# Performance work log

Measured on AMD Instinct MI355X. Metric: run time of the kernel, lower is better.

The kernel has to match this reference:

```python
import jax, jax.numpy as jnp
import numpy as np

N = 50000
E = 500000
R = 8
IN_DIM = 128
HID = 128
NUM_CLASSES = 16
NUM_GRAPHS = 64


def setup_inputs() -> dict:
    key = jax.random.key(0)
    ks = jax.random.split(key, 12)
    x = jax.random.normal(ks[0], (N, IN_DIM), dtype=jnp.float32)
    edge_index = jax.random.randint(ks[1], (2, E), 0, N)
    edge_type = jax.random.randint(ks[2], (E,), 0, R)
    batch = jnp.sort(jax.random.randint(ks[3], (N,), 0, NUM_GRAPHS))
    s = 1.0 / np.sqrt(IN_DIM)
    W1 = jax.random.uniform(ks[4], (R, IN_DIM, HID), minval=-s, maxval=s, dtype=jnp.float32)
    root1 = jax.random.uniform(ks[5], (IN_DIM, HID), minval=-s, maxval=s, dtype=jnp.float32)
    b1 = jnp.zeros((HID,), jnp.float32)
    s2 = 1.0 / np.sqrt(HID)
    W2 = jax.random.uniform(ks[6], (R, HID, HID), minval=-s2, maxval=s2, dtype=jnp.float32)
    root2 = jax.random.uniform(ks[7], (HID, HID), minval=-s2, maxval=s2, dtype=jnp.float32)
    b2 = jnp.zeros((HID,), jnp.float32)
    linW = jax.random.uniform(ks[8], (HID, NUM_CLASSES), minval=-s2, maxval=s2, dtype=jnp.float32)
    linb = jnp.zeros((NUM_CLASSES,), jnp.float32)
    return {"x": x, "edge_index": edge_index, "edge_type": edge_type, "batch": batch,
            "W1": W1, "root1": root1, "b1": b1, "W2": W2, "root2": root2, "b2": b2,
            "linW": linW, "linb": linb}


def rgcn_conv(x, src, dst, rel, W, root, b):
    # Per-relation transform of ALL nodes once: [R, N, H] (avoids per-edge weight gather)
    xW = jnp.einsum('nd,rdh->rnh', x, W)
    msg = xW[rel, src]                      # [E, H] gather per edge
    # PyG RGCNConv default aggr='mean': mean over neighbors per (dst, relation)
    seg = dst * R + rel                     # composite segment id
    cnt = jax.ops.segment_sum(jnp.ones((msg.shape[0],), msg.dtype), seg, num_segments=N * R)
    norm = 1.0 / jnp.maximum(cnt, 1.0)
    msg = msg * norm[seg][:, None]
    agg = jax.ops.segment_sum(msg, dst, num_segments=N)  # sum over relations folds in
    return agg + x @ root + b


def global_mean_pool(x, batch):
    sums = jax.ops.segment_sum(x, batch, num_segments=NUM_GRAPHS)
    cnt = jax.ops.segment_sum(jnp.ones((x.shape[0],), x.dtype), batch, num_segments=NUM_GRAPHS)
    return sums / jnp.maximum(cnt, 1.0)[:, None]


def reference(x, edge_index, edge_type, batch, W1, root1, b1, W2, root2, b2, linW, linb):
    src, dst = edge_index[0], edge_index[1]
    h = jax.nn.relu(rgcn_conv(x, src, dst, edge_type, W1, root1, b1))
    h = jax.nn.relu(rgcn_conv(h, src, dst, edge_type, W2, root2, b2))
    pooled = global_mean_pool(h, batch)     # [G, HID]
    return pooled @ linW + linb             # [G, NUM_CLASSES]
```

## Files before the change

### kernel.cpp

```cpp
#include <hip/hip_runtime.h>
#include <hip/hip_bf16.h>
#include <stdint.h>

#define N_NODES 50000
#define N_EDGES 500000
#define R_REL 8
#define HID 128
#define KIN 128
#define KOUT 1152
#define NUM_GRAPHS 64
#define NUM_CLASSES 16

#define BN 32
#define LDA 1160
#define NKC 36
#define NBLK 1563

typedef __attribute__((ext_vector_type(8))) short bf16x8;
typedef __attribute__((ext_vector_type(4))) float f32x4;

__device__ __forceinline__ uint16_t f2bf(float f) {
  uint32_t u = __float_as_uint(f);
  u += 0x7FFFu + ((u >> 16) & 1u);
  return (uint16_t)(u >> 16);
}
__device__ __forceinline__ float bf2f(uint32_t b) {
  return __uint_as_float(b << 16);
}
__device__ __forceinline__ uint32_t pack2bf(float a, float b) {
  return (uint32_t)f2bf(a) | ((uint32_t)f2bf(b) << 16);
}

#define HIST_B 1954
#define BND_B 196
#define PW_B 576
#define CVT_B 3125
__global__ __launch_bounds__(256) void k_prep(const int* __restrict__ ei, const int* __restrict__ et,
                                              int* __restrict__ deg,
                                              const int* __restrict__ batch,
                                              int* __restrict__ gs, int* __restrict__ ge,
                                              const float* __restrict__ W1, const float* __restrict__ root1,
                                              uint16_t* __restrict__ Wf1,
                                              const float* __restrict__ W2, const float* __restrict__ root2,
                                              uint16_t* __restrict__ Wf2,
                                              const float* __restrict__ x, uint16_t* __restrict__ xb) {
  int b = blockIdx.x;
  if (b < HIST_B) {
    int i = b * 256 + threadIdx.x;
    if (i < N_EDGES) atomicAdd(&deg[ei[N_EDGES + i]], 1);
    return;
  }
  b -= HIST_B;
  if (b < BND_B) {
    int i = b * 256 + threadIdx.x;
    if (i < N_NODES) {
      int g = batch[i];
      if (i == 0) gs[g] = 0;
      else { int pg = batch[i - 1]; if (pg != g) { ge[pg] = i; gs[g] = i; } }
      if (i == N_NODES - 1) ge[g] = N_NODES;
    }
    return;
  }
  b -= BND_B;
  if (b < 2 * PW_B) {
    const float* W    = (b < PW_B) ? W1 : W2;
    const float* root = (b < PW_B) ? root1 : root2;
    uint16_t*    Wf   = (b < PW_B) ? Wf1 : Wf2;
    int idx = (b % PW_B) * 256 + threadIdx.x;
    int e = idx & 7, L = (idx >> 3) & 63, f = idx >> 9;
    int quad = L >> 4, l16 = L & 15;
    int nt = f & 7, kc = f >> 3;
    int kk = kc * 32 + quad * 8 + e;
    int s = kk >> 7, k = kk & 127;
    int col = nt * 16 + l16;
    float v = (s < R_REL) ? W[((size_t)s * KIN + k) * HID + col] : root[(size_t)k * HID + col];
    Wf[idx] = f2bf(v);
    return;
  }
  b -= 2 * PW_B;
  {
    int i = b * 256 + threadIdx.x;
    const float4* p = (const float4*)x + (size_t)i * 2;
    float4 a = p[0], c = p[1];
    uint4 o;
    o.x = pack2bf(a.x, a.y); o.y = pack2bf(a.z, a.w);
    o.z = pack2bf(c.x, c.y); o.w = pack2bf(c.z, c.w);
    *(uint4*)(xb + (size_t)i * 8) = o;
  }
}

__global__ __launch_bounds__(256) void k_scan1(const int* __restrict__ deg, int* __restrict__ offs,
                                               int* __restrict__ bsum) {
  __shared__ int sh[256];
  int t = threadIdx.x;
  int base = blockIdx.x * 1024 + t * 4;
  int v[4]; int s = 0;
  #pragma unroll
  for (int i = 0; i < 4; ++i) { int idx = base + i; v[i] = (idx < N_NODES) ? deg[idx] : 0; s += v[i]; }
  sh[t] = s;
  __syncthreads();
  for (int d = 1; d < 256; d <<= 1) {
    int add = (t >= d) ? sh[t - d] : 0;
    __syncthreads();
    sh[t] += add;
    __syncthreads();
  }
  int run = sh[t] - s;
  if (t == 255) bsum[blockIdx.x] = sh[255];
  #pragma unroll
  for (int i = 0; i < 4; ++i) { int idx = base + i; if (idx < N_NODES) offs[idx] = run; run += v[i]; }
}

__global__ __launch_bounds__(512) void k_scan2(int* __restrict__ bsum, int nb) {
  __shared__ int sh[512];
  int t = threadIdx.x;
  int v = (t < nb) ? bsum[t] : 0;
  sh[t] = v;
  __syncthreads();
  for (int d = 1; d < 512; d <<= 1) {
    int add = (t >= d) ? sh[t - d] : 0;
    __syncthreads();
    sh[t] += add;
    __syncthreads();
  }
  if (t < nb) bsum[t] = sh[t] - v;
}

__global__ __launch_bounds__(256) void k_scan3(int* __restrict__ offs, int* __restrict__ nxt,
                                               const int* __restrict__ bsum) {
  int i = blockIdx.x * 256 + threadIdx.x;
  if (i < N_NODES) {
    int o = offs[i] + bsum[i >> 10];
    offs[i] = o;
    nxt[i] = o;
  }
  if (i == 0) offs[N_NODES] = N_EDGES;
}

__global__ __launch_bounds__(256) void k_scatter(const int* __restrict__ ei, const int* __restrict__ et,
                                                 int* __restrict__ nxt, uint32_t* __restrict__ epack) {
  int i = blockIdx.x * 256 + threadIdx.x;
  if (i < N_EDGES) {
    int rel = et[i];
    int key = ei[N_EDGES + i];
    int p = atomicAdd(&nxt[key], 1);
    epack[p] = (uint32_t)ei[i] | ((uint32_t)rel << 16);
  }
}

template<int MODE>
__global__ __launch_bounds__(512, 4) void k_fused(const uint16_t* __restrict__ hin,
                                                  const uint32_t* __restrict__ epack,
                                                  const int* __restrict__ offs,
                                                  const uint16_t* __restrict__ Wf,
                                                  const float* __restrict__ bias,
                                                  void* __restrict__ hout,
                                                  float* __restrict__ psum,
                                                  const int* __restrict__ batch) {
  __shared__ __align__(16) uint16_t As[BN * LDA];
  int t = threadIdx.x;
  int w = __builtin_amdgcn_readfirstlane(t >> 6);
  int L = t & 63;
  int quad = L >> 4, l16 = L & 15;
  int node0 = blockIdx.x * BN;

  {
    bf16x8 z = 0;
    #pragma unroll
    for (int i = 0; i < 9; ++i) ((bf16x8*)As)[i * 512 + t] = z;
    if (t < 32) ((bf16x8*)As)[9 * 512 + t] = z;
  }

  int offv = offs[min(node0 + min(L, 32), N_NODES)];

  const uint16_t* wp = Wf + (size_t)w * 512 + (size_t)L * 8;
  bf16x8 b0 = *(const bf16x8*)(wp);
  bf16x8 b1 = *(const bf16x8*)(wp + 1 * 4096);
  bf16x8 b2 = *(const bf16x8*)(wp + 2 * 4096);
  bf16x8 b3 = *(const bf16x8*)(wp + 3 * 4096);

  __syncthreads();

  {
    #pragma unroll
    for (int ni = 0; ni < 4; ++ni) {
      int n = node0 + w * 4 + ni;
      if (n < N_NODES)
        *(uint32_t*)(As + (w * 4 + ni) * LDA + R_REL * HID + L * 2) =
            *(const uint32_t*)(hin + (size_t)n * HID + L * 2);
    }

    float ax[8] = {0,0,0,0,0,0,0,0}, ay[8] = {0,0,0,0,0,0,0,0};
    int cn[8] = {0,0,0,0,0,0,0,0};

    int o0   = __builtin_amdgcn_readlane(offv, w * 4);
    int oEnd = __builtin_amdgcn_readlane(offv, w * 4 + 4);
    int curb = 0;
    int nbound = __builtin_amdgcn_readlane(offv, w * 4 + 1);

    auto FLUSH = [&](int nl) {
      uint16_t* Ar = As + nl * LDA;
      #pragma unroll
      for (int r = 0; r < 8; ++r) {
        if (cn[r]) {
          float iv = 1.0f / (float)cn[r];
          *(uint32_t*)(Ar + r * HID + L * 2) = pack2bf(ax[r] * iv, ay[r] * iv);
          ax[r] = 0.f; ay[r] = 0.f; cn[r] = 0;
        }
      }
    };

    #pragma unroll 1
    for (int g = o0; g < oEnd; g += 16) {
      int m = min(16, oEnd - g);
      uint32_t pvv[16], sv[16], vv[16];
      #pragma unroll
      for (int i = 0; i < 16; ++i) if (i < m) pvv[i] = epack[g + i];
      #pragma unroll
      for (int i = 0; i < 16; ++i) if (i < m) {
        uint32_t ps = __builtin_amdgcn_readfirstlane(pvv[i]);
        sv[i] = ps;
        const uint16_t* bp = hin + (size_t)(ps & 0xFFFFu) * HID;
        vv[i] = *(const uint32_t*)(bp + 2u * (uint32_t)L);
      }
      #pragma unroll
      for (int i = 0; i < 16; ++i) if (i < m) {
        int e = g + i;
        while (e >= nbound) {
          FLUSH(w * 4 + curb);
          ++curb;
          nbound = __builtin_amdgcn_readlane(offv, w * 4 + curb + 1);
        }
        uint32_t v = vv[i];
        float lo = bf2f(v & 0xFFFFu), hi = bf2f(v >> 16);
        uint32_t r = sv[i] >> 16;
        if (r < 4) {
          if (r < 2) { if (r == 0) { ax[0]+=lo; ay[0]+=hi; ++cn[0]; } else { ax[1]+=lo; ay[1]+=hi; ++cn[1]; } }
          else       { if (r == 2) { ax[2]+=lo; ay[2]+=hi; ++cn[2]; } else { ax[3]+=lo; ay[3]+=hi; ++cn[3]; } }
        } else {
          if (r < 6) { if (r == 4) { ax[4]+=lo; ay[4]+=hi; ++cn[4]; } else { ax[5]+=lo; ay[5]+=hi; ++cn[5]; } }
          else       { if (r == 6) { ax[6]+=lo; ay[6]+=hi; ++cn[6]; } else { ax[7]+=lo; ay[7]+=hi; ++cn[7]; } }
        }
      }
    }
    FLUSH(w * 4 + curb);
  }
  __syncthreads();

  f32x4 acc0 = (f32x4){0.f, 0.f, 0.f, 0.f};
  f32x4 acc1 = (f32x4){0.f, 0.f, 0.f, 0.f};
  const uint16_t* ap = As + l16 * LDA + quad * 8;

  bf16x8 a0 = *(const bf16x8*)(ap);
  bf16x8 a1 = *(const bf16x8*)(ap + 16 * LDA);

  #pragma unroll 1
  for (int kc = 0; kc < 32; kc += 4) {
    bf16x8 n0, n1, nb;
    n0 = *(const bf16x8*)(ap + (kc + 1) * 32);
    n1 = *(const bf16x8*)(ap + (kc + 1) * 32 + 16 * LDA);
    nb = *(const bf16x8*)(wp + (size_t)(kc + 4) * 4096);
    acc0 = __builtin_amdgcn_mfma_f32_16x16x32_bf16(a0, b0, acc0, 0, 0, 0);
    acc1 = __builtin_amdgcn_mfma_f32_16x16x32_bf16(a1, b0, acc1, 0, 0, 0);
    a0 = n0; a1 = n1; b0 = nb;
    n0 = *(const bf16x8*)(ap + (kc + 2) * 32);
    n1 = *(const bf16x8*)(ap + (kc + 2) * 32 + 16 * LDA);
    nb = *(const bf16x8*)(wp + (size_t)(kc + 5) * 4096);
    acc0 = __builtin_amdgcn_mfma_f32_16x16x32_bf16(a0, b1, acc0, 0, 0, 0);
    acc1 = __builtin_amdgcn_mfma_f32_16x16x32_bf16(a1, b1, acc1, 0, 0, 0);
    a0 = n0; a1 = n1; b1 = nb;
    n0 = *(const bf16x8*)(ap + (kc + 3) * 32);
    n1 = *(const bf16x8*)(ap + (kc + 3) * 32 + 16 * LDA);
    nb = *(const bf16x8*)(wp + (size_t)(kc + 6) * 4096);
    acc0 = __builtin_amdgcn_mfma_f32_16x16x32_bf16(a0, b2, acc0, 0, 0, 0);
    acc1 = __builtin_amdgcn_mfma_f32_16x16x32_bf16(a1, b2, acc1, 0, 0, 0);
    a0 = n0; a1 = n1; b2 = nb;
    n0 = *(const bf16x8*)(ap + (kc + 4) * 32);
    n1 = *(const bf16x8*)(ap + (kc + 4) * 32 + 16 * LDA);
    nb = *(const bf16x8*)(wp + (size_t)(kc + 7) * 4096);
    acc0 = __builtin_amdgcn_mfma_f32_16x16x32_bf16(a0, b3, acc0, 0, 0, 0);
    acc1 = __builtin_amdgcn_mfma_f32_16x16x32_bf16(a1, b3, acc1, 0, 0, 0);
    a0 = n0; a1 = n1; b3 = nb;
  }
  {
    bf16x8 n0, n1;
    n0 = *(const bf16x8*)(ap + 33 * 32);
    n1 = *(const bf16x8*)(ap + 33 * 32 + 16 * LDA);
    acc0 = __builtin_amdgcn_mfma_f32_16x16x32_bf16(a0, b0, acc0, 0, 0, 0);
    acc1 = __builtin_amdgcn_mfma_f32_16x16x32_bf16(a1, b0, acc1, 0, 0, 0);
    a0 = n0; a1 = n1;
    n0 = *(const bf16x8*)(ap + 34 * 32);
    n1 = *(const bf16x8*)(ap + 34 * 32 + 16 * LDA);
    acc0 = __builtin_amdgcn_mfma_f32_16x16x32_bf16(a0, b1, acc0, 0, 0, 0);
    acc1 = __builtin_amdgcn_mfma_f32_16x16x32_bf16(a1, b1, acc1, 0, 0, 0);
    a0 = n0; a1 = n1;
    n0 = *(const bf16x8*)(ap + 35 * 32);
    n1 = *(const bf16x8*)(ap + 35 * 32 + 16 * LDA);
    acc0 = __builtin_amdgcn_mfma_f32_16x16x32_bf16(a0, b2, acc0, 0, 0, 0);
    acc1 = __builtin_amdgcn_mfma_f32_16x16x32_bf16(a1, b2, acc1, 0, 0, 0);
    a0 = n0; a1 = n1;
    acc0 = __builtin_amdgcn_mfma_f32_16x16x32_bf16(a0, b3, acc0, 0, 0, 0);
    acc1 = __builtin_amdgcn_mfma_f32_16x16x32_bf16(a1, b3, acc1, 0, 0, 0);
  }

  int col = w * 16 + l16;
  float bv = bias[col];
  if (MODE == 0) {
    #pragma unroll
    for (int rg = 0; rg < 4; ++rg) {
      int row = node0 + quad * 4 + rg;
      if (row < N_NODES)
        ((uint16_t*)hout)[(size_t)row * HID + col] = f2bf(fmaxf(acc0[rg] + bv, 0.f));
    }
    #pragma unroll
    for (int rg = 0; rg < 4; ++rg) {
      int row = node0 + 16 + quad * 4 + rg;
      if (row < N_NODES)
        ((uint16_t*)hout)[(size_t)row * HID + col] = f2bf(fmaxf(acc1[rg] + bv, 0.f));
    }
  } else {
    bool fast = false;
    int gA = 0;
    if (node0 + BN <= N_NODES) {
      gA = batch[node0];
      int gB = batch[node0 + BN - 1];
      fast = (gA == gB);
    }
    if (fast) {
      float s = 0.f;
      #pragma unroll
      for (int rg = 0; rg < 4; ++rg) s += fmaxf(acc0[rg] + bv, 0.f);
      #pragma unroll
      for (int rg = 0; rg < 4; ++rg) s += fmaxf(acc1[rg] + bv, 0.f);
      s += __shfl_xor(s, 16);
      s += __shfl_xor(s, 32);
      if (quad == 0) atomicAdd(&psum[gA * HID + col], s);
    } else {
      int gp = -1; float run = 0.f;
      #pragma unroll
      for (int k = 0; k < 8; ++k) {
        int rg = k & 3;
        int row = node0 + (k >> 2) * 16 + quad * 4 + rg;
        float v = (k < 4) ? acc0[rg] : acc1[rg];
        if (row < N_NODES) {
          int gg = batch[row];
          if (gg != gp) {
            if (gp >= 0) atomicAdd(&psum[gp * HID + col], run);
            run = 0.f; gp = gg;
          }
          run += fmaxf(v + bv, 0.f);
        }
      }
      if (gp >= 0) atomicAdd(&psum[gp * HID + col], run);
    }
  }
}

__global__ __launch_bounds__(1024) void k_final(const float* __restrict__ psum,
                                                const int* __restrict__ gs, const int* __restrict__ ge,
                                                const float* __restrict__ linW, const float* __restrict__ linb,
                                                float* __restrict__ out) {
  int i = threadIdx.x;
  int g = i >> 4, c = i & 15;
  float inv = 1.f / fmaxf((float)(ge[g] - gs[g]), 1.f);
  float s = 0.f;
  #pragma unroll 8
  for (int k = 0; k < HID; ++k) s += psum[g * HID + k] * linW[k * NUM_CLASSES + c];
  out[i] = s * inv + linb[c];
}

extern "C" void kernel_launch(void* const* d_in, const int* in_sizes, int n_in,
                              void* d_out, int out_size, void* d_ws, size_t ws_size,
                              hipStream_t stream) {
  const float* x     = (const float*)d_in[0];
  const int*   ei    = (const int*)d_in[1];
  const int*   et    = (const int*)d_in[2];
  const int*   batch = (const int*)d_in[3];
  const float* W1    = (const float*)d_in[4];
  const float* root1 = (const float*)d_in[5];
  const float* b1    = (const float*)d_in[6];
  const float* W2    = (const float*)d_in[7];
  const float* root2 = (const float*)d_in[8];
  const float* b2    = (const float*)d_in[9];
  const float* linW  = (const float*)d_in[10];
  const float* linb  = (const float*)d_in[11];
  float* out = (float*)d_out;

  char* ws = (char*)d_ws;
  size_t off = 0;
  auto alloc = [&](size_t bytes) -> char* {
    char* p = ws + off;
    off += (bytes + 255) & ~(size_t)255;
    return p;
  };
  int*      deg   = (int*)alloc((size_t)N_NODES * 4);
  int*      gb    = (int*)alloc(2 * NUM_GRAPHS * 4);
  float*    psum  = (float*)alloc((size_t)NUM_GRAPHS * HID * 4);
  size_t zbytes = (((size_t)N_NODES * 4 + 255) & ~(size_t)255) + 512 + (size_t)NUM_GRAPHS * HID * 4;
  int*      gs    = gb;
  int*      ge    = gb + NUM_GRAPHS;
  int*      offs  = (int*)alloc((size_t)(N_NODES + 1) * 4);
  int*      nxt   = (int*)alloc((size_t)N_NODES * 4);
  int*      bsum  = (int*)alloc(512 * 4);
  uint32_t* epack = (uint32_t*)alloc((size_t)N_EDGES * 4);
  uint16_t* Wf1   = (uint16_t*)alloc((size_t)KOUT * KIN * 2);
  uint16_t* Wf2   = (uint16_t*)alloc((size_t)KOUT * KIN * 2);
  uint16_t* xb    = (uint16_t*)alloc((size_t)N_NODES * HID * 2);
  uint16_t* h1b   = (uint16_t*)alloc((size_t)N_NODES * HID * 2);

  hipMemsetAsync(deg, 0, zbytes, stream);

  int nb = (N_NODES + 1023) / 1024;
  k_prep<<<HIST_B + BND_B + 2 * PW_B + CVT_B, 256, 0, stream>>>(
      ei, et, deg, batch, gs, ge, W1, root1, Wf1, W2, root2, Wf2, x, xb);
  k_scan1<<<nb, 256, 0, stream>>>(deg, offs, bsum);
  k_scan2<<<1, 512, 0, stream>>>(bsum, nb);
  k_scan3<<<(N_NODES + 255) / 256, 256, 0, stream>>>(offs, nxt, bsum);
  k_scatter<<<(N_EDGES + 255) / 256, 256, 0, stream>>>(ei, et, nxt, epack);

  k_fused<0><<<NBLK, 512, 0, stream>>>(xb,  epack, offs, Wf1, b1, h1b, nullptr, nullptr);
  k_fused<1><<<NBLK, 512, 0, stream>>>(h1b, epack, offs, Wf2, b2, nullptr, psum, batch);

  k_final<<<1, 1024, 0, stream>>>(psum, gs, ge, linW, linb, out);
}
```

Baseline: 316.7 us.

## Balance edge aggregation across waves with LDS float atomics and split-K MFMA

Measured after the change: 1.033 ms. 3.26x slower.

```diff
diff --git a/kernel.cpp b/kernel.cpp
--- a/kernel.cpp
+++ b/kernel.cpp
@@ -13,7 +13,6 @@
 
 #define BN 32
 #define LDA 1160
-#define NKC 36
 #define NBLK 1563
 
 typedef __attribute__((ext_vector_type(8))) short bf16x8;
@@ -30,10 +29,11 @@
 __device__ __forceinline__ uint32_t pack2bf(float a, float b) {
   return (uint32_t)f2bf(a) | ((uint32_t)f2bf(b) << 16);
 }
+#define MFMA(a, b, c) __builtin_amdgcn_mfma_f32_16x16x32_bf16((a), (b), (c), 0, 0, 0)
 
 #define HIST_B 1954
 #define BND_B 196
-#define PW_B 576
+#define WP_B 72
 #define CVT_B 3125
 __global__ __launch_bounds__(256) void k_prep(const int* __restrict__ ei, const int* __restrict__ et,
                                               int* __restrict__ deg,
@@ -45,14 +45,15 @@
                                               uint16_t* __restrict__ Wf2,
                                               const float* __restrict__ x, uint16_t* __restrict__ xb) {
   int b = blockIdx.x;
+  int t = threadIdx.x;
   if (b < HIST_B) {
-    int i = b * 256 + threadIdx.x;
+    int i = b * 256 + t;
     if (i < N_EDGES) atomicAdd(&deg[ei[N_EDGES + i]], 1);
     return;
   }
   b -= HIST_B;
   if (b < BND_B) {
-    int i = b * 256 + threadIdx.x;
+    int i = b * 256 + t;
     if (i < N_NODES) {
       int g = batch[i];
       if (i == 0) gs[g] = 0;
@@ -62,24 +63,47 @@
     return;
   }
   b -= BND_B;
-  if (b < 2 * PW_B) {
-    const float* W    = (b < PW_B) ? W1 : W2;
-    const float* root = (b < PW_B) ? root1 : root2;
-    uint16_t*    Wf   = (b < PW_B) ? Wf1 : Wf2;
-    int idx = (b % PW_B) * 256 + threadIdx.x;
-    int e = idx & 7, L = (idx >> 3) & 63, f = idx >> 9;
-    int quad = L >> 4, l16 = L & 15;
-    int nt = f & 7, kc = f >> 3;
-    int kk = kc * 32 + quad * 8 + e;
-    int s = kk >> 7, k = kk & 127;
-    int col = nt * 16 + l16;
-    float v = (s < R_REL) ? W[((size_t)s * KIN + k) * HID + col] : root[(size_t)k * HID + col];
-    Wf[idx] = f2bf(v);
+  if (b < WP_B) {
+    __shared__ float lw[32 * 129];
+    const float* W    = (b < 36) ? W1 : W2;
+    const float* root = (b < 36) ? root1 : root2;
+    uint16_t*    Wf   = (b < 36) ? Wf1 : Wf2;
+    int kc = (b < 36) ? b : b - 36;
+    #pragma unroll
+    for (int j = 0; j < 4; ++j) {
+      int fi = j * 256 + t;
+      int row = fi >> 5, c4 = fi & 31;
+      int kk = kc * 32 + row;
+      int s = kk >> 7, k = kk & 127;
+      const float* src = (s < R_REL) ? (W + ((size_t)s * KIN + k) * HID) : (root + (size_t)k * HID);
+      float4 v = *(const float4*)(src + c4 * 4);
+      lw[row * 129 + c4 * 4 + 0] = v.x;
+      lw[row * 129 + c4 * 4 + 1] = v.y;
+      lw[row * 129 + c4 * 4 + 2] = v.z;
+      lw[row * 129 + c4 * 4 + 3] = v.w;
+    }
+    __syncthreads();
+    #pragma unroll
+    for (int p = 0; p < 2; ++p) {
+      int slot = p * 256 + t;
+      int nt = slot >> 6, L = slot & 63;
+      int quad = L >> 4, l16 = L & 15;
+      uint16_t tmp[8];
+      #pragma unroll
+      for (int e = 0; e < 8; ++e)
+        tmp[e] = f2bf(lw[(quad * 8 + e) * 129 + nt * 16 + l16]);
+      uint4 o;
+      o.x = (uint32_t)tmp[0] | ((uint32_t)tmp[1] << 16);
+      o.y = (uint32_t)tmp[2] | ((uint32_t)tmp[3] << 16);
+      o.z = (uint32_t)tmp[4] | ((uint32_t)tmp[5] << 16);
+      o.w = (uint32_t)tmp[6] | ((uint32_t)tmp[7] << 16);
+      *(uint4*)(Wf + ((size_t)(kc * 8 + nt) * 512 + (size_t)L * 8)) = o;
+    }
     return;
   }
-  b -= 2 * PW_B;
+  b -= WP_B;
   {
-    int i = b * 256 + threadIdx.x;
+    int i = b * 256 + t;
     const float4* p = (const float4*)x + (size_t)i * 2;
     float4 a = p[0], c = p[1];
     uint4 o;
@@ -142,216 +166,210 @@
   int i = blockIdx.x * 256 + threadIdx.x;
   if (i < N_EDGES) {
     int rel = et[i];
-    int key = ei[N_EDGES + i];
-    int p = atomicAdd(&nxt[key], 1);
-    epack[p] = (uint32_t)ei[i] | ((uint32_t)rel << 16);
+    int dst = ei[N_EDGES + i];
+    int p = atomicAdd(&nxt[dst], 1);
+    epack[p] = (uint32_t)ei[i] | ((uint32_t)rel << 16) | ((uint32_t)(dst & 31) << 19);
   }
 }
 
 template<int MODE>
-__global__ __launch_bounds__(512, 4) void k_fused(const uint16_t* __restrict__ hin,
-                                                  const uint32_t* __restrict__ epack,
-                                                  const int* __restrict__ offs,
-                                                  const uint16_t* __restrict__ Wf,
-                                                  const float* __restrict__ bias,
-                                                  void* __restrict__ hout,
-                                                  float* __restrict__ psum,
-                                                  const int* __restrict__ batch) {
-  __shared__ __align__(16) uint16_t As[BN * LDA];
+__global__ __launch_bounds__(1024, 4) void k_fused(const uint16_t* __restrict__ hin,
+                                                   const uint32_t* __restrict__ epack,
+                                                   const int* __restrict__ offs,
+                                                   const uint16_t* __restrict__ Wf,
+                                                   const float* __restrict__ bias,
+                                                   void* __restrict__ hout,
+                                                   float* __restrict__ psum,
+                                                   const int* __restrict__ batch) {
+  __shared__ __align__(16) float Af[BN * LDA + 256];
+  uint16_t* As = (uint16_t*)Af;
+  float* cnt = Af + BN * LDA;
+  float* scratch = (float*)((char*)Af + (size_t)BN * LDA * 2);
+
   int t = threadIdx.x;
   int w = __builtin_amdgcn_readfirstlane(t >> 6);
   int L = t & 63;
   int quad = L >> 4, l16 = L & 15;
   int node0 = blockIdx.x * BN;
+  int nt = w & 7, kh = w >> 3;
+
+  const uint16_t* wpk = Wf + ((size_t)(kh * 18 * 8 + nt)) * 512 + (size_t)L * 8;
+  bf16x8 b0 = *(const bf16x8*)(wpk);
+  bf16x8 b1 = *(const bf16x8*)(wpk + 4096);
 
   {
-    bf16x8 z = 0;
+    f32x4 z = {0.f, 0.f, 0.f, 0.f};
     #pragma unroll
-    for (int i = 0; i < 9; ++i) ((bf16x8*)As)[i * 512 + t] = z;
-    if (t < 32) ((bf16x8*)As)[9 * 512 + t] = z;
-  }
-
-  int offv = offs[min(node0 + min(L, 32), N_NODES)];
-
-  const uint16_t* wp = Wf + (size_t)w * 512 + (size_t)L * 8;
-  bf16x8 b0 = *(const bf16x8*)(wp);
-  bf16x8 b1 = *(const bf16x8*)(wp + 1 * 4096);
-  bf16x8 b2 = *(const bf16x8*)(wp + 2 * 4096);
-  bf16x8 b3 = *(const bf16x8*)(wp + 3 * 4096);
-
+    for (int j = 0; j < 8; ++j) {
+      int fi = j * 1024 + t;
+      int r = fi >> 8, k4 = fi & 255;
+      *(f32x4*)(Af + (size_t)r * LDA + k4 * 4) = z;
+    }
+    if (t < 256) cnt[t] = 0.f;
+    int r = t >> 5, d0 = (t & 31) * 4;
+    int n = node0 + r;
+    f32x4 rv = {0.f, 0.f, 0.f, 0.f};
+    if (n < N_NODES) {
+      uint32_t u0 = *(const uint32_t*)(hin + (size_t)n * HID + d0);
+      uint32_t u1 = *(const uint32_t*)(hin + (size_t)n * HID + d0 + 2);
+      rv[0] = bf2f(u0 & 0xFFFFu); rv[1] = bf2f(u0 >> 16);
+      rv[2] = bf2f(u1 & 0xFFFFu); rv[3] = bf2f(u1 >> 16);
+    }
+    *(f32x4*)(Af + (size_t)r * LDA + R_REL * HID + d0) = rv;
+  }
   __syncthreads();
 
   {
-    #pragma unroll
-    for (int ni = 0; ni < 4; ++ni) {
-      int n = node0 + w * 4 + ni;
-      if (n < N_NODES)
-        *(uint32_t*)(As + (w * 4 + ni) * LDA + R_REL * HID + L * 2) =
-            *(const uint32_t*)(hin + (size_t)n * HID + L * 2);
-    }
-
-    float ax[8] = {0,0,0,0,0,0,0,0}, ay[8] = {0,0,0,0,0,0,0,0};
-    int cn[8] = {0,0,0,0,0,0,0,0};
-
-    int o0   = __builtin_amdgcn_readlane(offv, w * 4);
-    int oEnd = __builtin_amdgcn_readlane(offv, w * 4 + 4);
-    int curb = 0;
-    int nbound = __builtin_amdgcn_readlane(offv, w * 4 + 1);
-
-    auto FLUSH = [&](int nl) {
-      uint16_t* Ar = As + nl * LDA;
-      #pragma unroll
-      for (int r = 0; r < 8; ++r) {
-        if (cn[r]) {
-          float iv = 1.0f / (float)cn[r];
-          *(uint32_t*)(Ar + r * HID + L * 2) = pack2bf(ax[r] * iv, ay[r] * iv);
-          ax[r] = 0.f; ay[r] = 0.f; cn[r] = 0;
-        }
-      }
-    };
-
+    int s0 = offs[node0];
+    int s1 = offs[min(node0 + BN, N_NODES)];
+    int ce = s1 - s0;
+    int e0 = s0 + ((ce * w) >> 4);
+    int e1 = s0 + ((ce * (w + 1)) >> 4);
+    int lsel = L & 15;
+    uint32_t pv = epack[e0 + lsel];
     #pragma unroll 1
-    for (int g = o0; g < oEnd; g += 16) {
-      int m = min(16, oEnd - g);
-      uint32_t pvv[16], sv[16], vv[16];
-      #pragma unroll
-      for (int i = 0; i < 16; ++i) if (i < m) pvv[i] = epack[g + i];
+    for (int g = e0; g < e1; g += 16) {
+      uint32_t pc = pv;
+      int m = min(16, e1 - g);
+      pv = epack[g + 16 + lsel];
+      uint32_t vv[16], sv[16];
       #pragma unroll
       for (int i = 0; i < 16; ++i) if (i < m) {
-        uint32_t ps = __builtin_amdgcn_readfirstlane(pvv[i]);
-        sv[i] = ps;
-        const uint16_t* bp = hin + (size_t)(ps & 0xFFFFu) * HID;
-        vv[i] = *(const uint32_t*)(bp + 2u * (uint32_t)L);
+        uint32_t s = (uint32_t)__builtin_amdgcn_readlane((int)pc, i);
+        sv[i] = s;
+        vv[i] = *(const uint32_t*)(hin + (size_t)(s & 0xFFFFu) * HID + 2u * (uint32_t)L);
       }
       #pragma unroll
       for (int i = 0; i < 16; ++i) if (i < m) {
-        int e = g + i;
-        while (e >= nbound) {
-          FLUSH(w * 4 + curb);
-          ++curb;
-          nbound = __builtin_amdgcn_readlane(offv, w * 4 + curb + 1);
+        uint32_t s = sv[i];
+        int rel = (int)((s >> 16) & 7u);
+        int loc = (int)(s >> 19);
+        float* slab = Af + (size_t)loc * LDA + rel * HID + 2 * L;
+        uint32_t v = vv[i];
+        atomicAdd(slab, bf2f(v & 0xFFFFu));
+        atomicAdd(slab + 1, bf2f(v >> 16));
+        if (L == 0) atomicAdd(&cnt[loc * 8 + rel], 1.0f);
+      }
+    }
+  }
+  __syncthreads();
+
+  {
+    f32x4 st[9];
+    #pragma unroll
+    for (int j = 0; j < 9; ++j) {
+      int fi = j * 1024 + t;
+      int r = fi / 288, k4 = fi - r * 288;
+      st[j] = *(const f32x4*)(Af + (size_t)r * LDA + k4 * 4);
+    }
+    __syncthreads();
+    #pragma unroll
+    for (int j = 0; j < 9; ++j) {
+      int fi = j * 1024 + t;
+      int r = fi / 288, k4 = fi - r * 288;
+      int rel = k4 >> 5;
+      float inv = 1.0f;
+      if (rel < R_REL) inv = 1.0f / fmaxf(cnt[r * 8 + rel], 1.0f);
+      f32x4 v = st[j];
+      uint2 o;
+      o.x = pack2bf(v[0] * inv, v[1] * inv);
+      o.y = pack2bf(v[2] * inv, v[3] * inv);
+      *(uint2*)(As + (size_t)r * LDA + k4 * 4) = o;
+    }
+  }
+  __syncthreads();
+
+  f32x4 acc0 = {0.f, 0.f, 0.f, 0.f};
+  f32x4 acc1 = {0.f, 0.f, 0.f, 0.f};
+  {
+    const uint16_t* apk = As + (size_t)l16 * LDA + quad * 8 + kh * 18 * 32;
+    bf16x8 a00 = *(const bf16x8*)(apk);
+    bf16x8 a01 = *(const bf16x8*)(apk + 16 * LDA);
+    #pragma unroll 1
+    for (int kc = 0; kc < 16; kc += 2) {
+      bf16x8 nb0 = *(const bf16x8*)(wpk + (size_t)(kc + 2) * 4096);
+      bf16x8 na0 = *(const bf16x8*)(apk + (kc + 1) * 32);
+      bf16x8 na1 = *(const bf16x8*)(apk + (kc + 1) * 32 + 16 * LDA);
+      acc0 = MFMA(a00, b0, acc0);
+      acc1 = MFMA(a01, b0, acc1);
+      b0 = nb0;
+      bf16x8 nb1 = *(const bf16x8*)(wpk + (size_t)(kc + 3) * 4096);
+      bf16x8 ma0 = *(const bf16x8*)(apk + (kc + 2) * 32);
+      bf16x8 ma1 = *(const bf16x8*)(apk + (kc + 2) * 32 + 16 * LDA);
+      acc0 = MFMA(na0, b1, acc0);
+      acc1 = MFMA(na1, b1, acc1);
+      b1 = nb1; a00 = ma0; a01 = ma1;
+    }
+    bf16x8 ta0 = *(const bf16x8*)(apk + 17 * 32);
+    bf16x8 ta1 = *(const bf16x8*)(apk + 17 * 32 + 16 * LDA);
+    acc0 = MFMA(a00, b0, acc0);
+    acc1 = MFMA(a01, b0, acc1);
+    acc0 = MFMA(ta0, b1, acc0);
+    acc1 = MFMA(ta1, b1, acc1);
+  }
+
+  if (kh == 1) {
+    float* sp = scratch + (size_t)(nt * 2) * 256 + L * 4;
+    *(f32x4*)(sp) = acc0;
+    *(f32x4*)(sp + 256) = acc1;
+  }
+  __syncthreads();
+  if (kh == 0) {
+    const float* sp = scratch + (size_t)(nt * 2) * 256 + L * 4;
+    f32x4 o0 = *(const f32x4*)(sp);
+    f32x4 o1 = *(const f32x4*)(sp + 256);
+    acc0 += o0;
+    acc1 += o1;
+    int col = nt * 16 + l16;
+    float bv = bias[col];
+    if (MODE == 0) {
+      #pragma unroll
+      for (int rg = 0; rg < 4; ++rg) {
+        int row = node0 + quad * 4 + rg;
+        if (row < N_NODES)
+          ((uint16_t*)hout)[(size_t)row * HID + col] = f2bf(fmaxf(acc0[rg] + bv, 0.f));
+      }
+      #pragma unroll
+      for (int rg = 0; rg < 4; ++rg) {
+        int row = node0 + 16 + quad * 4 + rg;
+        if (row < N_NODES)
+          ((uint16_t*)hout)[(size_t)row * HID + col] = f2bf(fmaxf(acc1[rg] + bv, 0.f));
+      }
+    } else {
+      bool fast = false;
+      int gA = 0;
+      if (node0 + BN <= N_NODES) {
+        gA = batch[node0];
+        int gB = batch[node0 + BN - 1];
+        fast = (gA == gB);
+      }
+      if (fast) {
+        float s = 0.f;
+        #pragma unroll
+        for (int rg = 0; rg < 4; ++rg) s += fmaxf(acc0[rg] + bv, 0.f);
+        #pragma unroll
+        for (int rg = 0; rg < 4; ++rg) s += fmaxf(acc1[rg] + bv, 0.f);
+        s += __shfl_xor(s, 16);
+        s += __shfl_xor(s, 32);
+        if (quad == 0) atomicAdd(&psum[gA * HID + col], s);
+      } else {
+        int gp = -1; float run = 0.f;
+        #pragma unroll
+        for (int k = 0; k < 8; ++k) {
+          int rg = k & 3;
+          int row = node0 + (k >> 2) * 16 + quad * 4 + rg;
+          float v = (k < 4) ? acc0[rg] : acc1[rg];
+          if (row < N_NODES) {
+            int gg = batch[row];
+            if (gg != gp) {
+              if (gp >= 0) atomicAdd(&psum[gp * HID + col], run);
+              run = 0.f; gp = gg;
+            }
+            run += fmaxf(v + bv, 0.f);
+          }
         }
-        uint32_t v = vv[i];
-        float lo = bf2f(v & 0xFFFFu), hi = bf2f(v >> 16);
-        uint32_t r = sv[i] >> 16;
-        if (r < 4) {
-          if (r < 2) { if (r == 0) { ax[0]+=lo; ay[0]+=hi; ++cn[0]; } else { ax[1]+=lo; ay[1]+=hi; ++cn[1]; } }
-          else       { if (r == 2) { ax[2]+=lo; ay[2]+=hi; ++cn[2]; } else { ax[3]+=lo; ay[3]+=hi; ++cn[3]; } }
-        } else {
-          if (r < 6) { if (r == 4) { ax[4]+=lo; ay[4]+=hi; ++cn[4]; } else { ax[5]+=lo; ay[5]+=hi; ++cn[5]; } }
-          else       { if (r == 6) { ax[6]+=lo; ay[6]+=hi; ++cn[6]; } else { ax[7]+=lo; ay[7]+=hi; ++cn[7]; } }
-        }
-      }
-    }
-    FLUSH(w * 4 + curb);
-  }
-  __syncthreads();
-
-  f32x4 acc0 = (f32x4){0.f, 0.f, 0.f, 0.f};
-  f32x4 acc1 = (f32x4){0.f, 0.f, 0.f, 0.f};
-  const uint16_t* ap = As + l16 * LDA + quad * 8;
-
-  bf16x8 a0 = *(const bf16x8*)(ap);
-  bf16x8 a1 = *(const bf16x8*)(ap + 16 * LDA);
-
-  #pragma unroll 1
-  for (int kc = 0; kc < 32; kc += 4) {
-    bf16x8 n0, n1, nb;
-    n0 = *(const bf16x8*)(ap + (kc + 1) * 32);
-    n1 = *(const bf16x8*)(ap + (kc + 1) * 32 + 16 * LDA);
-    nb = *(const bf16x8*)(wp + (size_t)(kc + 4) * 4096);
-    acc0 = __builtin_amdgcn_mfma_f32_16x16x32_bf16(a0, b0, acc0, 0, 0, 0);
-    acc1 = __builtin_amdgcn_mfma_f32_16x16x32_bf16(a1, b0, acc1, 0, 0, 0);
-    a0 = n0; a1 = n1; b0 = nb;
-    n0 = *(const bf16x8*)(ap + (kc + 2) * 32);
-    n1 = *(const bf16x8*)(ap + (kc + 2) * 32 + 16 * LDA);
-    nb = *(const bf16x8*)(wp + (size_t)(kc + 5) * 4096);
-    acc0 = __builtin_amdgcn_mfma_f32_16x16x32_bf16(a0, b1, acc0, 0, 0, 0);
-    acc1 = __builtin_amdgcn_mfma_f32_16x16x32_bf16(a1, b1, acc1, 0, 0, 0);
-    a0 = n0; a1 = n1; b1 = nb;
-    n0 = *(const bf16x8*)(ap + (kc + 3) * 32);
-    n1 = *(const bf16x8*)(ap + (kc + 3) * 32 + 16 * LDA);
-    nb = *(const bf16x8*)(wp + (size_t)(kc + 6) * 4096);
-    acc0 = __builtin_amdgcn_mfma_f32_16x16x32_bf16(a0, b2, acc0, 0, 0, 0);
-    acc1 = __builtin_amdgcn_mfma_f32_16x16x32_bf16(a1, b2, acc1, 0, 0, 0);
-    a0 = n0; a1 = n1; b2 = nb;
-    n0 = *(const bf16x8*)(ap + (kc + 4) * 32);
-    n1 = *(const bf16x8*)(ap + (kc + 4) * 32 + 16 * LDA);
-    nb = *(const bf16x8*)(wp + (size_t)(kc + 7) * 4096);
-    acc0 = __builtin_amdgcn_mfma_f32_16x16x32_bf16(a0, b3, acc0, 0, 0, 0);
-    acc1 = __builtin_amdgcn_mfma_f32_16x16x32_bf16(a1, b3, acc1, 0, 0, 0);
-    a0 = n0; a1 = n1; b3 = nb;
-  }
-  {
-    bf16x8 n0, n1;
-    n0 = *(const bf16x8*)(ap + 33 * 32);
-    n1 = *(const bf16x8*)(ap + 33 * 32 + 16 * LDA);
-    acc0 = __builtin_amdgcn_mfma_f32_16x16x32_bf16(a0, b0, acc0, 0, 0, 0);
-    acc1 = __builtin_amdgcn_mfma_f32_16x16x32_bf16(a1, b0, acc1, 0, 0, 0);
-    a0 = n0; a1 = n1;
-    n0 = *(const bf16x8*)(ap + 34 * 32);
-    n1 = *(const bf16x8*)(ap + 34 * 32 + 16 * LDA);
-    acc0 = __builtin_amdgcn_mfma_f32_16x16x32_bf16(a0, b1, acc0, 0, 0, 0);
-    acc1 = __builtin_amdgcn_mfma_f32_16x16x32_bf16(a1, b1, acc1, 0, 0, 0);
-    a0 = n0; a1 = n1;
-    n0 = *(const bf16x8*)(ap + 35 * 32);
-    n1 = *(const bf16x8*)(ap + 35 * 32 + 16 * LDA);
-    acc0 = __builtin_amdgcn_mfma_f32_16x16x32_bf16(a0, b2, acc0, 0, 0, 0);
-    acc1 = __builtin_amdgcn_mfma_f32_16x16x32_bf16(a1, b2, acc1, 0, 0, 0);
-    a0 = n0; a1 = n1;
-    acc0 = __builtin_amdgcn_mfma_f32_16x16x32_bf16(a0, b3, acc0, 0, 0, 0);
-    acc1 = __builtin_amdgcn_mfma_f32_16x16x32_bf16(a1, b3, acc1, 0, 0, 0);
-  }
-
-  int col = w * 16 + l16;
-  float bv = bias[col];
-  if (MODE == 0) {
-    #pragma unroll
-    for (int rg = 0; rg < 4; ++rg) {
-      int row = node0 + quad * 4 + rg;
-      if (row < N_NODES)
-        ((uint16_t*)hout)[(size_t)row * HID + col] = f2bf(fmaxf(acc0[rg] + bv, 0.f));
-    }
-    #pragma unroll
-    for (int rg = 0; rg < 4; ++rg) {
-      int row = node0 + 16 + quad * 4 + rg;
-      if (row < N_NODES)
-        ((uint16_t*)hout)[(size_t)row * HID + col] = f2bf(fmaxf(acc1[rg] + bv, 0.f));
-    }
-  } else {
-    bool fast = false;
-    int gA = 0;
-    if (node0 + BN <= N_NODES) {
-      gA = batch[node0];
-      int gB = batch[node0 + BN - 1];
-      fast = (gA == gB);
-    }
-    if (fast) {
-      float s = 0.f;
-      #pragma unroll
-      for (int rg = 0; rg < 4; ++rg) s += fmaxf(acc0[rg] + bv, 0.f);
-      #pragma unroll
-      for (int rg = 0; rg < 4; ++rg) s += fmaxf(acc1[rg] + bv, 0.f);
-      s += __shfl_xor(s, 16);
-      s += __shfl_xor(s, 32);
-      if (quad == 0) atomicAdd(&psum[gA * HID + col], s);
-    } else {
-      int gp = -1; float run = 0.f;
-      #pragma unroll
-      for (int k = 0; k < 8; ++k) {
-        int rg = k & 3;
-        int row = node0 + (k >> 2) * 16 + quad * 4 + rg;
-        float v = (k < 4) ? acc0[rg] : acc1[rg];
-        if (row < N_NODES) {
-          int gg = batch[row];
-          if (gg != gp) {
-            if (gp >= 0) atomicAdd(&psum[gp * HID + col], run);
-            run = 0.f; gp = gg;
-          }
-          run += fmaxf(v + bv, 0.f);
-        }
-      }
-      if (gp >= 0) atomicAdd(&psum[gp * HID + col], run);
+        if (gp >= 0) atomicAdd(&psum[gp * HID + col], run);
+      }
     }
   }
 }
@@ -402,7 +420,7 @@
   int*      offs  = (int*)alloc((size_t)(N_NODES + 1) * 4);
   int*      nxt   = (int*)alloc((size_t)N_NODES * 4);
   int*      bsum  = (int*)alloc(512 * 4);
-  uint32_t* epack = (uint32_t*)alloc((size_t)N_EDGES * 4);
+  uint32_t* epack = (uint32_t*)alloc((size_t)(N_EDGES + 64) * 4);
   uint16_t* Wf1   = (uint16_t*)alloc((size_t)KOUT * KIN * 2);
   uint16_t* Wf2   = (uint16_t*)alloc((size_t)KOUT * KIN * 2);
   uint16_t* xb    = (uint16_t*)alloc((size_t)N_NODES * HID * 2);
@@ -411,15 +429,15 @@
   hipMemsetAsync(deg, 0, zbytes, stream);
 
   int nb = (N_NODES + 1023) / 1024;
-  k_prep<<<HIST_B + BND_B + 2 * PW_B + CVT_B, 256, 0, stream>>>(
+  k_prep<<<HIST_B + BND_B + WP_B + CVT_B, 256, 0, stream>>>(
       ei, et, deg, batch, gs, ge, W1, root1, Wf1, W2, root2, Wf2, x, xb);
   k_scan1<<<nb, 256, 0, stream>>>(deg, offs, bsum);
   k_scan2<<<1, 512, 0, stream>>>(bsum, nb);
   k_scan3<<<(N_NODES + 255) / 256, 256, 0, stream>>>(offs, nxt, bsum);
   k_scatter<<<(N_EDGES + 255) / 256, 256, 0, stream>>>(ei, et, nxt, epack);
 
-  k_fused<0><<<NBLK, 512, 0, stream>>>(xb,  epack, offs, Wf1, b1, h1b, nullptr, nullptr);
-  k_fused<1><<<NBLK, 512, 0, stream>>>(h1b, epack, offs, Wf2, b2, nullptr, psum, batch);
+  k_fused<0><<<NBLK, 1024, 0, stream>>>(xb,  epack, offs, Wf1, b1, h1b, nullptr, nullptr);
+  k_fused<1><<<NBLK, 1024, 0, stream>>>(h1b, epack, offs, Wf2, b2, nullptr, psum, batch);
 
   k_final<<<1, 1024, 0, stream>>>(psum, gs, ge, linW, linb, out);
 }
```
